# Kernel tuning notes

Hardware: AMD Instinct MI355X
Metric: run time of the kernel (lower is better)

## Reference

```python
import jax, jax.numpy as jnp
import numpy as np

B, N, T, H = 32, 16, 64, 256


def setup_inputs() -> dict:
    key = jax.random.key(0)
    k1, k2, k3 = jax.random.split(key, 3)
    node_rnn_output = jax.random.normal(k1, (B, T, H), dtype=jnp.float32)
    neigh_rnn_output = jax.random.normal(k2, (B, N, T, H), dtype=jnp.float32)
    # neighbor counts in [1, N] to avoid divide-by-zero in 1/sqrt scaling
    neighbors_number = jax.random.randint(k3, (B,), 1, N + 1, dtype=jnp.int64)
    return {
        "node_rnn_output": node_rnn_output,
        "neigh_rnn_output": neigh_rnn_output,
        "neighbors_number": neighbors_number,
    }


def reference(node_rnn_output, neigh_rnn_output, neighbors_number):
    b, t, h = node_rnn_output.shape
    n = neigh_rnn_output.shape[1]
    # [B, N*T, H]
    flat_neigh = neigh_rnn_output.reshape(b, n * t, h)
    # repeat node output along time axis: [B, N*T, H]
    stacked_node = jnp.tile(node_rnn_output, (1, n, 1))
    # S = flat_neigh @ stacked_node^T : [B, N*T, N*T]
    S = jnp.einsum("bqh,bkh->bqk", flat_neigh, stacked_node)
    scale = jnp.sqrt(neighbors_number.astype(S.dtype))  # [B]
    S = S / scale[:, None, None]
    A = jax.nn.softmax(S, axis=-1)
    # dropout with p=0 (eval / reference) is identity
    W = A.sum(axis=1).reshape(b, n, t)  # [B, N, T]
    output = jnp.einsum("bqk,bkh->bqh", A, flat_neigh)  # [B, N*T, H]
    return (output, W)
```

## Files before the change

kernel.cpp:

```cpp
#include <hip/hip_runtime.h>

#define Bc  32
#define Nc  16
#define Tc  64
#define Hc  256
#define NTc 1024

typedef unsigned short u16;
using v8s = __attribute__((ext_vector_type(8))) short;
using v4f = __attribute__((ext_vector_type(4))) float;

static __device__ __forceinline__ u16 f2bf(float x) {
    unsigned u = __float_as_uint(x);
    unsigned r = u + 0x7fffu + ((u >> 16) & 1u);
    return (u16)(r >> 16);
}
static __device__ __forceinline__ float bf2f(u16 h) {
    return __uint_as_float(((unsigned)h) << 16);
}

__global__ __launch_bounds__(256) void prep_kernel(const float* __restrict__ neigh,
                                                   const float* __restrict__ node,
                                                   u16* __restrict__ MT,
                                                   u16* __restrict__ NH,
                                                   u16* __restrict__ NL,
                                                   float* __restrict__ Wsum) {
    __shared__ float Ls[16][68];
    int bk = blockIdx.x, tid = threadIdx.x;

    if (bk < 512) {
        int b  = bk >> 4;
        int h0 = ((bk >> 2) & 3) << 6;
        int t0 = (bk & 3) << 4;
        int t  = tid >> 4;
        int h4 = tid & 15;
        const float4* p = (const float4*)(neigh + ((size_t)(b * Nc * Tc) + (t0 + t)) * Hc + h0) + h4;
        float4 a = make_float4(0.f, 0.f, 0.f, 0.f);
#pragma unroll
        for (int i = 0; i < Nc; i++) {
            float4 v = p[(size_t)i * (Tc * Hc / 4)];
            a.x += v.x; a.y += v.y; a.z += v.z; a.w += v.w;
        }
        const float r = 1.0f / 16.0f;
        Ls[t][h4 * 4 + 0] = a.x * r;
        Ls[t][h4 * 4 + 1] = a.y * r;
        Ls[t][h4 * 4 + 2] = a.z * r;
        Ls[t][h4 * 4 + 3] = a.w * r;
        __syncthreads();
        int h  = tid >> 2;
        int t4 = tid & 3;
        ushort4 o;
        o.x = f2bf(Ls[t4 * 4 + 0][h]);
        o.y = f2bf(Ls[t4 * 4 + 1][h]);
        o.z = f2bf(Ls[t4 * 4 + 2][h]);
        o.w = f2bf(Ls[t4 * 4 + 3][h]);
        *(ushort4*)(MT + ((size_t)b * Hc + h0 + h) * Tc + t0 + t4 * 4) = o;
    } else {
        int b = bk - 512;
#pragma unroll
        for (int rep = 0; rep < 16; rep++) {
            int idx = rep * 256 + tid;
            int t = idx >> 6, c4 = idx & 63;
            size_t off = ((size_t)b * Tc + t) * Hc + c4 * 4;
            float4 v = *(const float4*)(node + off);
            ushort4 hs, ls;
            hs.x = f2bf(v.x); ls.x = f2bf(v.x - bf2f(hs.x));
            hs.y = f2bf(v.y); ls.y = f2bf(v.y - bf2f(hs.y));
            hs.z = f2bf(v.z); ls.z = f2bf(v.z - bf2f(hs.z));
            hs.w = f2bf(v.w); ls.w = f2bf(v.w - bf2f(hs.w));
            *(ushort4*)(NH + off) = hs;
            *(ushort4*)(NL + off) = ls;
        }
        if (tid < 64) Wsum[b * 64 + tid] = 0.f;
    }
}

__global__ __launch_bounds__(256, 2) void fused_kernel(const float* __restrict__ neigh,
                                                       const u16* __restrict__ NH,
                                                       const u16* __restrict__ NL,
                                                       const int* __restrict__ nbr,
                                                       const u16* __restrict__ MT,
                                                       float* __restrict__ out,
                                                       float* __restrict__ Wsum) {
    __shared__ u16 Ph[64][72];
    __shared__ float Wtmp[256];

    int b  = blockIdx.x >> 4;
    int i  = blockIdx.x & 15;
    int q0 = i << 6;

    int tid  = threadIdx.x;
    int w    = tid >> 6;
    int lane = tid & 63;
    int quad = lane >> 4;
    int c    = lane & 15;

    int nb = (nbr[1] == 0) ? nbr[2 * b] : nbr[b];
    float rscale = rsqrtf((float)nb);

    const float* Xrow = neigh + ((size_t)(b * Nc * Tc) + q0 + w * 16 + c) * Hc;
    const u16*   NHb  = NH + (size_t)b * Tc * Hc;
    const u16*   NLb  = NL + (size_t)b * Tc * Hc;
    const u16*   MTb  = MT + (size_t)b * Hc * Tc;

    v4f acc[4];
#pragma unroll
    for (int nt = 0; nt < 4; nt++)
#pragma unroll
        for (int rg = 0; rg < 4; rg++) acc[nt][rg] = 0.f;

#pragma unroll
    for (int ks = 0; ks < Hc; ks += 32) {
        float4 f0 = *(const float4*)(Xrow + ks + quad * 8);
        float4 f1 = *(const float4*)(Xrow + ks + quad * 8 + 4);
        v8s ah, al;
        {
            u16 h0 = f2bf(f0.x), h1 = f2bf(f0.y), h2 = f2bf(f0.z), h3 = f2bf(f0.w);
            u16 h4 = f2bf(f1.x), h5 = f2bf(f1.y), h6 = f2bf(f1.z), h7 = f2bf(f1.w);
            ah[0] = (short)h0; ah[1] = (short)h1; ah[2] = (short)h2; ah[3] = (short)h3;
            ah[4] = (short)h4; ah[5] = (short)h5; ah[6] = (short)h6; ah[7] = (short)h7;
            al[0] = (short)f2bf(f0.x - bf2f(h0)); al[1] = (short)f2bf(f0.y - bf2f(h1));
            al[2] = (short)f2bf(f0.z - bf2f(h2)); al[3] = (short)f2bf(f0.w - bf2f(h3));
            al[4] = (short)f2bf(f1.x - bf2f(h4)); al[5] = (short)f2bf(f1.y - bf2f(h5));
            al[6] = (short)f2bf(f1.z - bf2f(h6)); al[7] = (short)f2bf(f1.w - bf2f(h7));
        }
#pragma unroll
        for (int nt = 0; nt < 4; nt++) {
            size_t roff = (size_t)(nt * 16 + c) * Hc + ks + quad * 8;
            v8s bh = *(const v8s*)(NHb + roff);
            v8s bl = *(const v8s*)(NLb + roff);
            acc[nt] = __builtin_amdgcn_mfma_f32_16x16x32_bf16(ah, bh, acc[nt], 0, 0, 0);
            acc[nt] = __builtin_amdgcn_mfma_f32_16x16x32_bf16(ah, bl, acc[nt], 0, 0, 0);
            acc[nt] = __builtin_amdgcn_mfma_f32_16x16x32_bf16(al, bh, acc[nt], 0, 0, 0);
        }
    }

#pragma unroll
    for (int nt = 0; nt < 4; nt++)
#pragma unroll
        for (int rg = 0; rg < 4; rg++) acc[nt][rg] *= rscale;

#pragma unroll
    for (int rg = 0; rg < 4; rg++) {
        float m = fmaxf(fmaxf(acc[0][rg], acc[1][rg]), fmaxf(acc[2][rg], acc[3][rg]));
#pragma unroll
        for (int d = 1; d < 16; d <<= 1) m = fmaxf(m, __shfl_xor(m, d));
        float e0 = __expf(acc[0][rg] - m);
        float e1 = __expf(acc[1][rg] - m);
        float e2 = __expf(acc[2][rg] - m);
        float e3 = __expf(acc[3][rg] - m);
        float s = e0 + e1 + e2 + e3;
#pragma unroll
        for (int d = 1; d < 16; d <<= 1) s += __shfl_xor(s, d);
        float inv = 1.0f / s;
        acc[0][rg] = e0 * inv; acc[1][rg] = e1 * inv;
        acc[2][rg] = e2 * inv; acc[3][rg] = e3 * inv;
    }

#pragma unroll
    for (int nt = 0; nt < 4; nt++) {
        float cs = acc[nt][0] + acc[nt][1] + acc[nt][2] + acc[nt][3];
        cs += __shfl_xor(cs, 16);
        cs += __shfl_xor(cs, 32);
        if (quad == 0) Wtmp[w * 64 + nt * 16 + c] = cs;
    }

#pragma unroll
    for (int nt = 0; nt < 4; nt++)
#pragma unroll
        for (int rg = 0; rg < 4; rg++)
            Ph[w * 16 + quad * 4 + rg][nt * 16 + c] = f2bf(acc[nt][rg]);

    __syncthreads();

    if (tid < 64) {
        float s = Wtmp[tid] + Wtmp[64 + tid] + Wtmp[128 + tid] + Wtmp[192 + tid];
        atomicAdd(&Wsum[b * Tc + tid], s);
    }

    v8s pa0 = *(const v8s*)&Ph[w * 16 + c][quad * 8];
    v8s pa1 = *(const v8s*)&Ph[w * 16 + c][32 + quad * 8];

    float* ob = out + ((size_t)b * NTc + q0 + w * 16 + quad * 4) * Hc + c;
#pragma unroll
    for (int ht = 0; ht < 16; ht++) {
        const u16* mr = MTb + (size_t)(ht * 16 + c) * Tc;
        v8s b0 = *(const v8s*)(mr + quad * 8);
        v8s b1 = *(const v8s*)(mr + 32 + quad * 8);
        v4f oc;
        oc[0] = 0.f; oc[1] = 0.f; oc[2] = 0.f; oc[3] = 0.f;
        oc = __builtin_amdgcn_mfma_f32_16x16x32_bf16(pa0, b0, oc, 0, 0, 0);
        oc = __builtin_amdgcn_mfma_f32_16x16x32_bf16(pa1, b1, oc, 0, 0, 0);
#pragma unroll
        for (int rg = 0; rg < 4; rg++)
            ob[(size_t)rg * Hc + ht * 16] = oc[rg];
    }
}

__global__ __launch_bounds__(256) void wexp_kernel(const float* __restrict__ Wsum,
                                                   float* __restrict__ Wout) {
    int idx = blockIdx.x * 256 + threadIdx.x;
    int b = idx >> 10;
    int t = idx & 63;
    Wout[idx] = Wsum[b * Tc + t] * (1.0f / 16.0f);
}

extern "C" void kernel_launch(void* const* d_in, const int* in_sizes, int n_in,
                              void* d_out, int out_size, void* d_ws, size_t ws_size,
                              hipStream_t stream) {
    const float* node  = (const float*)d_in[0];
    const float* neigh = (const float*)d_in[1];
    const int*   nbr   = (const int*)d_in[2];

    float* out = (float*)d_out;

    u16* MTw = (u16*)d_ws;
    u16* NHw = MTw + (size_t)Bc * Hc * Tc;
    u16* NLw = NHw + (size_t)Bc * Tc * Hc;
    float* Ww = (float*)(NLw + (size_t)Bc * Tc * Hc);

    prep_kernel <<<544, 256, 0, stream>>>(neigh, node, MTw, NHw, NLw, Ww);
    fused_kernel<<<512, 256, 0, stream>>>(neigh, NHw, NLw, nbr, MTw, out, Ww);
    wexp_kernel <<<128, 256, 0, stream>>>(Ww, out + (size_t)Bc * NTc * Hc);
}
```

Measured before the change: 121.0 us.

## Pre-swizzle node and mean operands into MFMA fragment order for coalesced loads

The prep kernel now writes the bf16 hi/lo node split and the transposed neighbor mean directly in per-lane MFMA fragment order. The fused kernel can then load each B operand as one contiguous 16-byte chunk per lane, with consecutive lanes adjacent, instead of strided row gathers. The prep mean reduction is reorganised to one 16-column slab per block, leaving only half the threads doing the transposed write. The fused kernel's launch bounds drop the minimum-two-blocks hint, which may change register allocation and occupancy.

```diff
diff --git a/kernel.cpp b/kernel.cpp
--- a/kernel.cpp
+++ b/kernel.cpp
@@ -19,22 +19,25 @@
     return __uint_as_float(((unsigned)h) << 16);
 }
 
+#define NFRAG_NODE 2048
+#define NFRAG_MT   2048
+
 __global__ __launch_bounds__(256) void prep_kernel(const float* __restrict__ neigh,
                                                    const float* __restrict__ node,
-                                                   u16* __restrict__ MT,
-                                                   u16* __restrict__ NH,
-                                                   u16* __restrict__ NL,
+                                                   u16* __restrict__ MTf,
+                                                   u16* __restrict__ NHf,
+                                                   u16* __restrict__ NLf,
                                                    float* __restrict__ Wsum) {
-    __shared__ float Ls[16][68];
+    __shared__ float Ls[64][17];
     int bk = blockIdx.x, tid = threadIdx.x;
 
     if (bk < 512) {
         int b  = bk >> 4;
-        int h0 = ((bk >> 2) & 3) << 6;
-        int t0 = (bk & 3) << 4;
-        int t  = tid >> 4;
-        int h4 = tid & 15;
-        const float4* p = (const float4*)(neigh + ((size_t)(b * Nc * Tc) + (t0 + t)) * Hc + h0) + h4;
+        int hc = bk & 15;
+        int h0 = hc << 4;
+        int t  = tid >> 2;
+        int h4 = tid & 3;
+        const float4* p = (const float4*)(neigh + ((size_t)(b * Nc * Tc) + t) * Hc + h0) + h4;
         float4 a = make_float4(0.f, 0.f, 0.f, 0.f);
 #pragma unroll
         for (int i = 0; i < Nc; i++) {
@@ -47,41 +50,52 @@
         Ls[t][h4 * 4 + 2] = a.z * r;
         Ls[t][h4 * 4 + 3] = a.w * r;
         __syncthreads();
-        int h  = tid >> 2;
-        int t4 = tid & 3;
-        ushort4 o;
-        o.x = f2bf(Ls[t4 * 4 + 0][h]);
-        o.y = f2bf(Ls[t4 * 4 + 1][h]);
-        o.z = f2bf(Ls[t4 * 4 + 2][h]);
-        o.w = f2bf(Ls[t4 * 4 + 3][h]);
-        *(ushort4*)(MT + ((size_t)b * Hc + h0 + h) * Tc + t0 + t4 * 4) = o;
+        if (tid < 128) {
+            int ktb  = tid >> 6;
+            int lane = tid & 63;
+            int quad = lane >> 4;
+            int c    = lane & 15;
+            v8s o;
+#pragma unroll
+            for (int j = 0; j < 8; j++)
+                o[j] = (short)f2bf(Ls[ktb * 32 + quad * 8 + j][c]);
+            *(v8s*)(MTf + ((size_t)b * NFRAG_MT + (hc * 2 + ktb) * 64 + lane) * 8) = o;
+        }
     } else {
         int b = bk - 512;
 #pragma unroll
-        for (int rep = 0; rep < 16; rep++) {
-            int idx = rep * 256 + tid;
-            int t = idx >> 6, c4 = idx & 63;
-            size_t off = ((size_t)b * Tc + t) * Hc + c4 * 4;
-            float4 v = *(const float4*)(node + off);
-            ushort4 hs, ls;
-            hs.x = f2bf(v.x); ls.x = f2bf(v.x - bf2f(hs.x));
-            hs.y = f2bf(v.y); ls.y = f2bf(v.y - bf2f(hs.y));
-            hs.z = f2bf(v.z); ls.z = f2bf(v.z - bf2f(hs.z));
-            hs.w = f2bf(v.w); ls.w = f2bf(v.w - bf2f(hs.w));
-            *(ushort4*)(NH + off) = hs;
-            *(ushort4*)(NL + off) = ls;
+        for (int rep = 0; rep < 8; rep++) {
+            int f    = rep * 256 + tid;
+            int nt   = f >> 9;
+            int ksb  = (f >> 6) & 7;
+            int lane = f & 63;
+            int quad = lane >> 4;
+            int c    = lane & 15;
+            const float* src = node + ((size_t)b * Tc + nt * 16 + c) * Hc + ksb * 32 + quad * 8;
+            float4 f0 = *(const float4*)(src);
+            float4 f1 = *(const float4*)(src + 4);
+            v8s hs, ls;
+            float vin[8] = {f0.x, f0.y, f0.z, f0.w, f1.x, f1.y, f1.z, f1.w};
+#pragma unroll
+            for (int j = 0; j < 8; j++) {
+                u16 h = f2bf(vin[j]);
+                hs[j] = (short)h;
+                ls[j] = (short)f2bf(vin[j] - bf2f(h));
+            }
+            *(v8s*)(NHf + ((size_t)b * NFRAG_NODE + f) * 8) = hs;
+            *(v8s*)(NLf + ((size_t)b * NFRAG_NODE + f) * 8) = ls;
         }
         if (tid < 64) Wsum[b * 64 + tid] = 0.f;
     }
 }
 
-__global__ __launch_bounds__(256, 2) void fused_kernel(const float* __restrict__ neigh,
-                                                       const u16* __restrict__ NH,
-                                                       const u16* __restrict__ NL,
-                                                       const int* __restrict__ nbr,
-                                                       const u16* __restrict__ MT,
-                                                       float* __restrict__ out,
-                                                       float* __restrict__ Wsum) {
+__global__ __launch_bounds__(256) void fused_kernel(const float* __restrict__ neigh,
+                                                    const u16* __restrict__ NHf,
+                                                    const u16* __restrict__ NLf,
+                                                    const int* __restrict__ nbr,
+                                                    const u16* __restrict__ MTf,
+                                                    float* __restrict__ out,
+                                                    float* __restrict__ Wsum) {
     __shared__ u16 Ph[64][72];
     __shared__ float Wtmp[256];
 
@@ -99,9 +113,9 @@
     float rscale = rsqrtf((float)nb);
 
     const float* Xrow = neigh + ((size_t)(b * Nc * Tc) + q0 + w * 16 + c) * Hc;
-    const u16*   NHb  = NH + (size_t)b * Tc * Hc;
-    const u16*   NLb  = NL + (size_t)b * Tc * Hc;
-    const u16*   MTb  = MT + (size_t)b * Hc * Tc;
+    const u16*   NHb  = NHf + (size_t)b * NFRAG_NODE * 8 + lane * 8;
+    const u16*   NLb  = NLf + (size_t)b * NFRAG_NODE * 8 + lane * 8;
+    const u16*   MTb  = MTf + (size_t)b * NFRAG_MT   * 8 + lane * 8;
 
     v4f acc[4];
 #pragma unroll
@@ -110,25 +124,24 @@
         for (int rg = 0; rg < 4; rg++) acc[nt][rg] = 0.f;
 
 #pragma unroll
-    for (int ks = 0; ks < Hc; ks += 32) {
-        float4 f0 = *(const float4*)(Xrow + ks + quad * 8);
-        float4 f1 = *(const float4*)(Xrow + ks + quad * 8 + 4);
+    for (int ksb = 0; ksb < 8; ksb++) {
+        float4 f0 = *(const float4*)(Xrow + ksb * 32 + quad * 8);
+        float4 f1 = *(const float4*)(Xrow + ksb * 32 + quad * 8 + 4);
         v8s ah, al;
         {
-            u16 h0 = f2bf(f0.x), h1 = f2bf(f0.y), h2 = f2bf(f0.z), h3 = f2bf(f0.w);
-            u16 h4 = f2bf(f1.x), h5 = f2bf(f1.y), h6 = f2bf(f1.z), h7 = f2bf(f1.w);
-            ah[0] = (short)h0; ah[1] = (short)h1; ah[2] = (short)h2; ah[3] = (short)h3;
-            ah[4] = (short)h4; ah[5] = (short)h5; ah[6] = (short)h6; ah[7] = (short)h7;
-            al[0] = (short)f2bf(f0.x - bf2f(h0)); al[1] = (short)f2bf(f0.y - bf2f(h1));
-            al[2] = (short)f2bf(f0.z - bf2f(h2)); al[3] = (short)f2bf(f0.w - bf2f(h3));
-            al[4] = (short)f2bf(f1.x - bf2f(h4)); al[5] = (short)f2bf(f1.y - bf2f(h5));
-            al[6] = (short)f2bf(f1.z - bf2f(h6)); al[7] = (short)f2bf(f1.w - bf2f(h7));
+            float vin[8] = {f0.x, f0.y, f0.z, f0.w, f1.x, f1.y, f1.z, f1.w};
+#pragma unroll
+            for (int j = 0; j < 8; j++) {
+                u16 h = f2bf(vin[j]);
+                ah[j] = (short)h;
+                al[j] = (short)f2bf(vin[j] - bf2f(h));
+            }
         }
 #pragma unroll
         for (int nt = 0; nt < 4; nt++) {
-            size_t roff = (size_t)(nt * 16 + c) * Hc + ks + quad * 8;
-            v8s bh = *(const v8s*)(NHb + roff);
-            v8s bl = *(const v8s*)(NLb + roff);
+            size_t foff = (size_t)((nt * 8 + ksb) * 64) * 8;
+            v8s bh = *(const v8s*)(NHb + foff);
+            v8s bl = *(const v8s*)(NLb + foff);
             acc[nt] = __builtin_amdgcn_mfma_f32_16x16x32_bf16(ah, bh, acc[nt], 0, 0, 0);
             acc[nt] = __builtin_amdgcn_mfma_f32_16x16x32_bf16(ah, bl, acc[nt], 0, 0, 0);
             acc[nt] = __builtin_amdgcn_mfma_f32_16x16x32_bf16(al, bh, acc[nt], 0, 0, 0);
@@ -184,9 +197,8 @@
     float* ob = out + ((size_t)b * NTc + q0 + w * 16 + quad * 4) * Hc + c;
 #pragma unroll
     for (int ht = 0; ht < 16; ht++) {
-        const u16* mr = MTb + (size_t)(ht * 16 + c) * Tc;
-        v8s b0 = *(const v8s*)(mr + quad * 8);
-        v8s b1 = *(const v8s*)(mr + 32 + quad * 8);
+        v8s b0 = *(const v8s*)(MTb + (size_t)((ht * 2 + 0) * 64) * 8);
+        v8s b1 = *(const v8s*)(MTb + (size_t)((ht * 2 + 1) * 64) * 8);
         v4f oc;
         oc[0] = 0.f; oc[1] = 0.f; oc[2] = 0.f; oc[3] = 0.f;
         oc = __builtin_amdgcn_mfma_f32_16x16x32_bf16(pa0, b0, oc, 0, 0, 0);
@@ -215,9 +227,9 @@
     float* out = (float*)d_out;
 
     u16* MTw = (u16*)d_ws;
-    u16* NHw = MTw + (size_t)Bc * Hc * Tc;
-    u16* NLw = NHw + (size_t)Bc * Tc * Hc;
-    float* Ww = (float*)(NLw + (size_t)Bc * Tc * Hc);
+    u16* NHw = MTw + (size_t)Bc * NFRAG_MT * 8;
+    u16* NLw = NHw + (size_t)Bc * NFRAG_NODE * 8;
+    float* Ww = (float*)(NLw + (size_t)Bc * NFRAG_NODE * 8);
 
     prep_kernel <<<544, 256, 0, stream>>>(neigh, node, MTw, NHw, NLw, Ww);
     fused_kernel<<<512, 256, 0, stream>>>(neigh, NHw, NLw, nbr, MTw, out, Ww);
```

Measured after the change: 116.5 us. -3.7%, faster.
